# Optimization experiments

Measured on AMD Instinct MI355X. Metric: run time of the kernel, lower is better.

Reference implementation:

```python
import jax, jax.numpy as jnp
import numpy as np

T = 4  # message-passing steps (hparams['T'])
D = 64  # link_state_dim
RU = 256  # readout_units


def setup_inputs() -> dict:
    key = jax.random.key(0)
    ks = jax.random.split(key, 12)
    num_edges = 100000
    n_pairs = 1600000
    link_state = jax.random.normal(ks[0], (num_edges, D), dtype=jnp.float32)
    first_critic = jax.random.randint(ks[1], (n_pairs,), 0, num_edges)
    second_critic = jax.random.randint(ks[2], (n_pairs,), 0, num_edges)
    s = 0.05
    return {
        'link_state': link_state,
        'first_critic': first_critic,
        'second_critic': second_critic,
        'num_edges_critic': num_edges,
        'W_msg': jax.random.normal(ks[3], (2 * D, D), dtype=jnp.float32) * s,
        'b_msg': jnp.zeros((D,), dtype=jnp.float32),
        'gru_kernel': jax.random.normal(ks[4], (D, 3 * D), dtype=jnp.float32) * s,
        'gru_rkernel': jax.random.normal(ks[5], (D, 3 * D), dtype=jnp.float32) * s,
        'gru_bias': jnp.zeros((2, 3 * D), dtype=jnp.float32),  # reset_after=True: [input_bias, recurrent_bias]
        'W1': jax.random.normal(ks[6], (D, RU), dtype=jnp.float32) * s,
        'b1': jnp.zeros((RU,), dtype=jnp.float32),
        'W2': jax.random.normal(ks[7], (RU, RU), dtype=jnp.float32) * s,
        'b2': jnp.zeros((RU,), dtype=jnp.float32),
        'W3': jax.random.normal(ks[8], (RU, 1), dtype=jnp.float32) * s,
        'b3': jnp.zeros((1,), dtype=jnp.float32),
    }


def _gru_cell(x, h, kernel, rkernel, bias):
    # Keras GRUCell, reset_after=True
    mx = x @ kernel + bias[0]          # [E, 3D]
    mi = h @ rkernel + bias[1]         # [E, 3D]
    z = jax.nn.sigmoid(mx[:, :D] + mi[:, :D])
    r = jax.nn.sigmoid(mx[:, D:2 * D] + mi[:, D:2 * D])
    hh = jnp.tanh(mx[:, 2 * D:] + r * mi[:, 2 * D:])
    return z * h + (1.0 - z) * hh


def reference(link_state, first_critic, second_critic, num_edges_critic,
              W_msg, b_msg, gru_kernel, gru_rkernel, gru_bias,
              W1, b1, W2, b2, W3, b3):
    for _ in range(T):
        main_nodes = link_state[first_critic]        # [P, D] gather
        neigh_nodes = link_state[second_critic]      # [P, D] gather
        nodes_concat = jnp.concatenate([main_nodes, neigh_nodes], axis=1)  # [P, 2D]
        msg = jax.nn.selu(nodes_concat @ W_msg + b_msg)                    # [P, D]
        agg = jax.ops.segment_sum(msg, second_critic, num_segments=num_edges_critic)  # [E, D]
        link_state = _gru_cell(agg, link_state, gru_kernel, gru_rkernel, gru_bias)
    # tf.reduce_sum([link_state], axis=1): stack -> [1, E, D], sum over E -> [1, D]
    g = jnp.sum(link_state, axis=0, keepdims=True)   # [1, D]
    h1 = jax.nn.selu(g @ W1 + b1)
    h2 = jax.nn.selu(h1 @ W2 + b2)
    return h2 @ W3 + b3                              # [1, 1]
```

## Files before the change

### kernel.cpp

```cpp
#include <hip/hip_runtime.h>
#include <hip/hip_bf16.h>

#define D 64
#define TSTEPS 4

__device__ __forceinline__ float selu_f(float x) {
  const float sc = 1.0507009873554805f;
  const float scal = 1.7580993408473766f;
  return x > 0.f ? sc * x : scal * (__expf(x) - 1.f);
}
__device__ __forceinline__ float sigm_f(float x) {
  return 1.f / (1.f + __expf(-x));
}
__device__ __forceinline__ float tanh_f(float x) {
  return 1.f - 2.f / (__expf(2.f * x) + 1.f);
}
__device__ __forceinline__ unsigned short f2bf(float x) {
  union { float f; unsigned u; } v; v.f = x;
  unsigned r = v.u + 0x7fff + ((v.u >> 16) & 1);
  return (unsigned short)(r >> 16);
}
__device__ __forceinline__ float bf2f(unsigned short x) {
  union { unsigned u; float f; } v; v.u = ((unsigned)x) << 16;
  return v.f;
}

__global__ void k_setup(int* __restrict__ counts, float* __restrict__ g, int E) {
  for (int i = blockIdx.x * blockDim.x + threadIdx.x; i < E; i += gridDim.x * blockDim.x)
    counts[i] = 0;
  int t = blockIdx.x * blockDim.x + threadIdx.x;
  if (t < D) g[t] = 0.f;
}

__global__ void k_hist(const int* __restrict__ sec, int* counts, int P) {
  int i = blockIdx.x * blockDim.x + threadIdx.x;
  if (i < P) atomicAdd(&counts[sec[i]], 1);
}

__global__ void k_scan(const int* __restrict__ counts, int* __restrict__ offsets,
                       int* __restrict__ cursor, int E, int P) {
  __shared__ int lds[1024];
  int t = threadIdx.x;
  int per = (E + 1023) >> 10;
  int lo = t * per, hi = min(lo + per, E);
  int s = 0;
  for (int i = lo; i < hi; ++i) s += counts[i];
  lds[t] = s;
  __syncthreads();
  for (int d = 1; d < 1024; d <<= 1) {
    int v = (t >= d) ? lds[t - d] : 0;
    __syncthreads();
    lds[t] += v;
    __syncthreads();
  }
  int run = (t == 0) ? 0 : lds[t - 1];
  for (int i = lo; i < hi; ++i) {
    int c = counts[i];
    offsets[i] = run;
    cursor[i] = run;
    run += c;
  }
  if (t == 1023) offsets[E] = P;
}

__global__ void k_scatter(const int* __restrict__ fst, const int* __restrict__ sec,
                          int* cursor, int* __restrict__ sorted_first, int P) {
  int i = blockIdx.x * blockDim.x + threadIdx.x;
  if (i < P) {
    int e = sec[i];
    int pos = atomicAdd(&cursor[e], 1);
    sorted_first[pos] = fst[i];
  }
}

__global__ void k_prep(const float* __restrict__ Wmsg,
                       const float* __restrict__ gk, const float* __restrict__ grk,
                       const float* __restrict__ gb,
                       float* __restrict__ Wuv, float* __restrict__ Wg, float* __restrict__ bg) {
  int i = blockIdx.x * blockDim.x + threadIdx.x;
  if (i < 64 * 128) {
    int k = i >> 7, c = i & 127;
    Wuv[i] = (c < 64) ? Wmsg[k * 64 + c] : Wmsg[(64 + k) * 64 + (c - 64)];
  }
  if (i < 128 * 256) {
    int r = i >> 8, c = i & 255;
    float v;
    if (r < 64) {
      v = (c < 192) ? gk[r * 192 + c] : 0.f;
    } else {
      int rr = r - 64;
      if (c < 128) v = grk[rr * 192 + c];
      else if (c < 192) v = 0.f;
      else v = grk[rr * 192 + (c - 64)];
    }
    Wg[i] = v;
  }
  if (i < 256) {
    float v;
    if (i < 128) v = gb[i] + gb[192 + i];
    else if (i < 192) v = gb[i];
    else v = gb[i + 128];
    bg[i] = v;
  }
}

template <int UV16>
__global__ __launch_bounds__(256) void k_uv(const float* __restrict__ h,
                                            const float* __restrict__ Wuv,
                                            const float* __restrict__ bmsg,
                                            void* __restrict__ UVp, int E) {
  __shared__ float As[32 * 65];
  int t = threadIdx.x;
  int base = blockIdx.x * 32;
  for (int q = t; q < 32 * 16; q += 256) {
    int row = q >> 4, k4 = (q & 15) << 2;
    float4 v = make_float4(0.f, 0.f, 0.f, 0.f);
    if (base + row < E)
      v = *reinterpret_cast<const float4*>(h + (size_t)(base + row) * 64 + k4);
    As[row * 65 + k4 + 0] = v.x;
    As[row * 65 + k4 + 1] = v.y;
    As[row * 65 + k4 + 2] = v.z;
    As[row * 65 + k4 + 3] = v.w;
  }
  __syncthreads();
  int ct = t & 31, eg = t >> 5;
  int c0 = ct * 4;
  float4 binit = make_float4(0.f, 0.f, 0.f, 0.f);
  if (c0 >= 64) binit = *reinterpret_cast<const float4*>(bmsg + (c0 - 64));
  float4 acc[4];
  acc[0] = binit; acc[1] = binit; acc[2] = binit; acc[3] = binit;
#pragma unroll 8
  for (int k = 0; k < 64; ++k) {
    float4 bv = *reinterpret_cast<const float4*>(Wuv + k * 128 + c0);
#pragma unroll
    for (int j = 0; j < 4; ++j) {
      float a = As[(eg + j * 8) * 65 + k];
      acc[j].x += a * bv.x; acc[j].y += a * bv.y;
      acc[j].z += a * bv.z; acc[j].w += a * bv.w;
    }
  }
#pragma unroll
  for (int j = 0; j < 4; ++j) {
    int e = base + eg + j * 8;
    if (e < E) {
      if constexpr (UV16) {
        ushort4 s;
        s.x = f2bf(acc[j].x); s.y = f2bf(acc[j].y);
        s.z = f2bf(acc[j].z); s.w = f2bf(acc[j].w);
        *reinterpret_cast<ushort4*>((unsigned short*)UVp + (size_t)e * 128 + c0) = s;
      } else {
        *reinterpret_cast<float4*>((float*)UVp + (size_t)e * 128 + c0) = acc[j];
      }
    }
  }
}

template <int UV16, int AGG16>
__global__ __launch_bounds__(256) void k_pair(const void* __restrict__ UVp,
                                              const int* __restrict__ offsets,
                                              const int* __restrict__ sorted_first,
                                              void* __restrict__ aggp, int E) {
  int w = (blockIdx.x << 2) + (threadIdx.x >> 6);
  if (w >= E) return;
  int c = threadIdx.x & 63;
  const float* UV32 = (const float*)UVp;
  const unsigned short* UV16p = (const unsigned short*)UVp;
  float base;
  if constexpr (UV16) base = bf2f(UV16p[(size_t)w * 128 + 64 + c]);
  else                base = UV32[(size_t)w * 128 + 64 + c];
  int i = offsets[w], end = offsets[w + 1];
  float acc = 0.f;
  for (; i + 3 < end; i += 4) {
    int f0 = sorted_first[i];
    int f1 = sorted_first[i + 1];
    int f2 = sorted_first[i + 2];
    int f3 = sorted_first[i + 3];
    float u0, u1, u2, u3;
    if constexpr (UV16) {
      u0 = bf2f(UV16p[(size_t)f0 * 128 + c]);
      u1 = bf2f(UV16p[(size_t)f1 * 128 + c]);
      u2 = bf2f(UV16p[(size_t)f2 * 128 + c]);
      u3 = bf2f(UV16p[(size_t)f3 * 128 + c]);
    } else {
      u0 = UV32[(size_t)f0 * 128 + c];
      u1 = UV32[(size_t)f1 * 128 + c];
      u2 = UV32[(size_t)f2 * 128 + c];
      u3 = UV32[(size_t)f3 * 128 + c];
    }
    acc += selu_f(u0 + base);
    acc += selu_f(u1 + base);
    acc += selu_f(u2 + base);
    acc += selu_f(u3 + base);
  }
  for (; i < end; ++i) {
    int f0 = sorted_first[i];
    float u;
    if constexpr (UV16) u = bf2f(UV16p[(size_t)f0 * 128 + c]);
    else                u = UV32[(size_t)f0 * 128 + c];
    acc += selu_f(u + base);
  }
  if constexpr (AGG16)
    ((unsigned short*)aggp)[(size_t)w * 64 + c] = f2bf(acc);
  else
    ((float*)aggp)[(size_t)w * 64 + c] = acc;
}

template <int UV16, int AGG16>
__global__ __launch_bounds__(256) void k_gru(const void* __restrict__ aggp,
                                             const float* __restrict__ h_in,
                                             float* __restrict__ h_out,
                                             const float* __restrict__ Wg,
                                             const float* __restrict__ bg,
                                             const float* __restrict__ Wuv,
                                             const float* __restrict__ bmsg,
                                             void* __restrict__ UVp,
                                             float* __restrict__ g,
                                             int E, int write_uv, int accum_g) {
  __shared__ float As[32 * 129];
  __shared__ float Ms[32 * 257];
  __shared__ float red[256];
  int t = threadIdx.x;
  int base = blockIdx.x * 32;

  for (int q = t; q < 32 * 32; q += 256) {
    int row = q >> 5, c4 = (q & 31) << 2;
    int e = base + row;
    float4 v = make_float4(0.f, 0.f, 0.f, 0.f);
    if (e < E) {
      if (c4 < 64) {
        if constexpr (AGG16) {
          ushort4 s = *reinterpret_cast<const ushort4*>(
              (const unsigned short*)aggp + (size_t)e * 64 + c4);
          v = make_float4(bf2f(s.x), bf2f(s.y), bf2f(s.z), bf2f(s.w));
        } else {
          v = *reinterpret_cast<const float4*>((const float*)aggp + (size_t)e * 64 + c4);
        }
      } else {
        v = *reinterpret_cast<const float4*>(h_in + (size_t)e * 64 + (c4 - 64));
      }
    }
    As[row * 129 + c4 + 0] = v.x;
    As[row * 129 + c4 + 1] = v.y;
    As[row * 129 + c4 + 2] = v.z;
    As[row * 129 + c4 + 3] = v.w;
  }
  __syncthreads();

  {
    int wv = t >> 6;
    int lane = t & 63;
    int ct8 = lane & 7;
    int rg = lane >> 3;
    int c0 = wv * 64 + ct8 * 8;
    int kbeg = (wv == 3) ? 64 : 0;
    int kend = (wv == 2) ? 64 : 128;
    float4 b0 = *reinterpret_cast<const float4*>(bg + c0);
    float4 b1 = *reinterpret_cast<const float4*>(bg + c0 + 4);
    float4 acc0[4], acc1[4];
#pragma unroll
    for (int j = 0; j < 4; ++j) { acc0[j] = b0; acc1[j] = b1; }
#pragma unroll 4
    for (int k = kbeg; k < kend; ++k) {
      float4 bv0 = *reinterpret_cast<const float4*>(Wg + k * 256 + c0);
      float4 bv1 = *reinterpret_cast<const float4*>(Wg + k * 256 + c0 + 4);
#pragma unroll
      for (int j = 0; j < 4; ++j) {
        float a = As[(rg + j * 8) * 129 + k];
        acc0[j].x += a * bv0.x; acc0[j].y += a * bv0.y;
        acc0[j].z += a * bv0.z; acc0[j].w += a * bv0.w;
        acc1[j].x += a * bv1.x; acc1[j].y += a * bv1.y;
        acc1[j].z += a * bv1.z; acc1[j].w += a * bv1.w;
      }
    }
#pragma unroll
    for (int j = 0; j < 4; ++j) {
      float* m = Ms + (rg + j * 8) * 257 + c0;
      m[0] = acc0[j].x; m[1] = acc0[j].y; m[2] = acc0[j].z; m[3] = acc0[j].w;
      m[4] = acc1[j].x; m[5] = acc1[j].y; m[6] = acc1[j].z; m[7] = acc1[j].w;
    }
  }
  __syncthreads();

  float gsum = 0.f;
#pragma unroll
  for (int j = 0; j < 8; ++j) {
    int u = t + 256 * j;
    int e = u >> 6, c = u & 63;
    int ge = base + e;
    float mz = Ms[e * 257 + c];
    float mr = Ms[e * 257 + 64 + c];
    float mx2 = Ms[e * 257 + 128 + c];
    float mi2 = Ms[e * 257 + 192 + c];
    float hold = As[e * 129 + 64 + c];
    float z = sigm_f(mz);
    float r = sigm_f(mr);
    float hh = tanh_f(mx2 + r * mi2);
    float hn = z * hold + (1.f - z) * hh;
    if (ge < E) {
      h_out[(size_t)ge * 64 + c] = hn;
    } else {
      hn = 0.f;
    }
    As[e * 129 + 64 + c] = hn;
    gsum += hn;
  }
  __syncthreads();

  if (write_uv) {
    int ct = t & 31, eg = t >> 5;
    int c0 = ct * 4;
    float4 binit = make_float4(0.f, 0.f, 0.f, 0.f);
    if (c0 >= 64) binit = *reinterpret_cast<const float4*>(bmsg + (c0 - 64));
    float4 acc[4];
    acc[0] = binit; acc[1] = binit; acc[2] = binit; acc[3] = binit;
#pragma unroll 8
    for (int k = 0; k < 64; ++k) {
      float4 bv = *reinterpret_cast<const float4*>(Wuv + k * 128 + c0);
#pragma unroll
      for (int j = 0; j < 4; ++j) {
        float a = As[(eg + j * 8) * 129 + 64 + k];
        acc[j].x += a * bv.x; acc[j].y += a * bv.y;
        acc[j].z += a * bv.z; acc[j].w += a * bv.w;
      }
    }
#pragma unroll
    for (int j = 0; j < 4; ++j) {
      int e = base + eg + j * 8;
      if (e < E) {
        if constexpr (UV16) {
          ushort4 s;
          s.x = f2bf(acc[j].x); s.y = f2bf(acc[j].y);
          s.z = f2bf(acc[j].z); s.w = f2bf(acc[j].w);
          *reinterpret_cast<ushort4*>((unsigned short*)UVp + (size_t)e * 128 + c0) = s;
        } else {
          *reinterpret_cast<float4*>((float*)UVp + (size_t)e * 128 + c0) = acc[j];
        }
      }
    }
  }

  if (accum_g) {
    red[t] = gsum;
    __syncthreads();
    if (t < 64) atomicAdd(&g[t], red[t] + red[t + 64] + red[t + 128] + red[t + 192]);
  }
}

__global__ __launch_bounds__(256) void k_mlp(const float* __restrict__ g,
                                             const float* __restrict__ W1, const float* __restrict__ b1,
                                             const float* __restrict__ W2, const float* __restrict__ b2,
                                             const float* __restrict__ W3, const float* __restrict__ b3,
                                             float* __restrict__ out) {
  __shared__ float gs[64];
  __shared__ float h1[256];
  __shared__ float h2[256];
  __shared__ float red[256];
  int t = threadIdx.x;
  if (t < 64) gs[t] = g[t];
  __syncthreads();
  float acc = b1[t];
#pragma unroll
  for (int k = 0; k < 64; ++k) acc += gs[k] * W1[k * 256 + t];
  h1[t] = selu_f(acc);
  __syncthreads();
  acc = b2[t];
#pragma unroll 8
  for (int k = 0; k < 256; ++k) acc += h1[k] * W2[k * 256 + t];
  h2[t] = selu_f(acc);
  __syncthreads();
  red[t] = h2[t] * W3[t];
  __syncthreads();
  for (int d = 128; d > 0; d >>= 1) {
    if (t < d) red[t] += red[t + d];
    __syncthreads();
  }
  if (t == 0) out[0] = red[0] + b3[0];
}

extern "C" void kernel_launch(void* const* d_in, const int* in_sizes, int n_in,
                              void* d_out, int out_size, void* d_ws, size_t ws_size,
                              hipStream_t stream) {
  const float* ls   = (const float*)d_in[0];
  const int*   fst  = (const int*)d_in[1];
  const int*   sec  = (const int*)d_in[2];
  const float* Wmsg = (const float*)d_in[4];
  const float* bmsg = (const float*)d_in[5];
  const float* gk   = (const float*)d_in[6];
  const float* grk  = (const float*)d_in[7];
  const float* gb   = (const float*)d_in[8];
  const float* W1   = (const float*)d_in[9];
  const float* b1   = (const float*)d_in[10];
  const float* W2   = (const float*)d_in[11];
  const float* b2   = (const float*)d_in[12];
  const float* W3   = (const float*)d_in[13];
  const float* b3   = (const float*)d_in[14];
  int E = in_sizes[0] / D;
  int P = in_sizes[1];
  float* out = (float*)d_out;
  (void)n_in; (void)out_size;

  auto total_need = [&](int uv16, int agg16) -> size_t {
    size_t o = 0;
    auto add = [&](size_t b) { o = (o + b + 255) & ~(size_t)255; };
    add((size_t)E * 64 * 4);
    add((size_t)E * 128 * (uv16 ? 2 : 4));
    add((size_t)E * 64 * (agg16 ? 2 : 4));
    add(((size_t)E + 1) * 4);
    add((size_t)E * 4);
    add((size_t)P * 4);
    add(64 * 128 * 4);
    add(128 * 256 * 4);
    add(256 * 4);
    add(64 * 4);
    return o;
  };
  int uv16 = 0, agg16 = 0;
  if (total_need(0, 0) > ws_size) { uv16 = 1; }
  if (uv16 && total_need(1, 0) > ws_size) { agg16 = 1; }

  char* ws = (char*)d_ws;
  size_t off = 0;
  auto alloc = [&](size_t bytes) {
    void* p = ws + off;
    off = (off + bytes + 255) & ~(size_t)255;
    return p;
  };
  float* h            = (float*)alloc((size_t)E * 64 * 4);
  void*  UV           = alloc((size_t)E * 128 * (uv16 ? 2 : 4));
  void*  agg          = alloc((size_t)E * 64 * (agg16 ? 2 : 4));
  int*   offsets      = (int*)alloc(((size_t)E + 1) * 4);
  int*   counts       = (int*)alloc((size_t)E * 4);
  int*   cursor       = counts;
  int*   sorted_first = (int*)alloc((size_t)P * 4);
  float* Wuv          = (float*)alloc(64 * 128 * 4);
  float* Wg           = (float*)alloc(128 * 256 * 4);
  float* bg           = (float*)alloc(256 * 4);
  float* g            = (float*)alloc(64 * 4);

  k_setup<<<512, 256, 0, stream>>>(counts, g, E);
  k_hist<<<(P + 255) / 256, 256, 0, stream>>>(sec, counts, P);
  k_scan<<<1, 1024, 0, stream>>>(counts, offsets, cursor, E, P);
  k_scatter<<<(P + 255) / 256, 256, 0, stream>>>(fst, sec, cursor, sorted_first, P);
  k_prep<<<128, 256, 0, stream>>>(Wmsg, gk, grk, gb, Wuv, Wg, bg);

  int gemm_blocks = (E + 31) / 32;
  int pair_blocks = (E + 3) / 4;

  if (!uv16) {
    k_uv<0><<<gemm_blocks, 256, 0, stream>>>(ls, Wuv, bmsg, UV, E);
    for (int it = 0; it < TSTEPS; ++it) {
      const float* hin = (it == 0) ? ls : h;
      int last = (it == TSTEPS - 1);
      k_pair<0, 0><<<pair_blocks, 256, 0, stream>>>(UV, offsets, sorted_first, agg, E);
      k_gru<0, 0><<<gemm_blocks, 256, 0, stream>>>(agg, hin, h, Wg, bg, Wuv, bmsg, UV, g,
                                                   E, !last, last);
    }
  } else if (!agg16) {
    k_uv<1><<<gemm_blocks, 256, 0, stream>>>(ls, Wuv, bmsg, UV, E);
    for (int it = 0; it < TSTEPS; ++it) {
      const float* hin = (it == 0) ? ls : h;
      int last = (it == TSTEPS - 1);
      k_pair<1, 0><<<pair_blocks, 256, 0, stream>>>(UV, offsets, sorted_first, agg, E);
      k_gru<1, 0><<<gemm_blocks, 256, 0, stream>>>(agg, hin, h, Wg, bg, Wuv, bmsg, UV, g,
                                                   E, !last, last);
    }
  } else {
    k_uv<1><<<gemm_blocks, 256, 0, stream>>>(ls, Wuv, bmsg, UV, E);
    for (int it = 0; it < TSTEPS; ++it) {
      const float* hin = (it == 0) ? ls : h;
      int last = (it == TSTEPS - 1);
      k_pair<1, 1><<<pair_blocks, 256, 0, stream>>>(UV, offsets, sorted_first, agg, E);
      k_gru<1, 1><<<gemm_blocks, 256, 0, stream>>>(agg, hin, h, Wg, bg, Wuv, bmsg, UV, g,
                                                   E, !last, last);
    }
  }
  k_mlp<<<1, 256, 0, stream>>>(g, W1, b1, W2, b2, W3, b3, out);
}
```

Baseline: 1.349 ms.

## Fuse pair aggregation into GRU kernel, parallelize scan, force bf16 UV

Adds a fused kernel that computes each block's segment-summed messages straight into shared memory and then runs the GRU and next-step UV projection, with UV double-buffered across steps so the separate agg buffer and per-step pair kernel launch go away. The single-block serial scan becomes a three-pass multi-block scan, and wave-uniform indices are marked with readfirstlane so they live in scalar registers. UV and agg are now always stored as bf16 instead of choosing by workspace size, which lowers precision in the fp32 cases. The last step skips writing h, and a memset replaces the setup kernel. The fused kernel uses about 50KB of shared memory per block and leaves one wave per edge row, which may reduce occupancy and latency hiding for the random gathers.

```diff
diff --git a/kernel.cpp b/kernel.cpp
--- a/kernel.cpp
+++ b/kernel.cpp
@@ -25,42 +25,81 @@
   return v.f;
 }
 
-__global__ void k_setup(int* __restrict__ counts, float* __restrict__ g, int E) {
-  for (int i = blockIdx.x * blockDim.x + threadIdx.x; i < E; i += gridDim.x * blockDim.x)
-    counts[i] = 0;
-  int t = blockIdx.x * blockDim.x + threadIdx.x;
-  if (t < D) g[t] = 0.f;
-}
-
 __global__ void k_hist(const int* __restrict__ sec, int* counts, int P) {
   int i = blockIdx.x * blockDim.x + threadIdx.x;
   if (i < P) atomicAdd(&counts[sec[i]], 1);
 }
 
-__global__ void k_scan(const int* __restrict__ counts, int* __restrict__ offsets,
-                       int* __restrict__ cursor, int E, int P) {
+__global__ __launch_bounds__(256) void k_scan1(const int* __restrict__ counts,
+                                               int* __restrict__ bsums, int E) {
+  __shared__ int red[256];
+  int b = blockIdx.x, t = threadIdx.x;
+  int i0 = b * 1024 + t * 4;
+  int s = 0;
+  if (i0 + 3 < E) {
+    int4 v = *reinterpret_cast<const int4*>(counts + i0);
+    s = v.x + v.y + v.z + v.w;
+  } else {
+#pragma unroll
+    for (int j = 0; j < 4; ++j) { int i = i0 + j; if (i < E) s += counts[i]; }
+  }
+  red[t] = s;
+  __syncthreads();
+  for (int d = 128; d > 0; d >>= 1) {
+    if (t < d) red[t] += red[t + d];
+    __syncthreads();
+  }
+  if (t == 0) bsums[b] = red[0];
+}
+
+__global__ __launch_bounds__(1024) void k_scan2(int* __restrict__ bsums, int NB) {
   __shared__ int lds[1024];
   int t = threadIdx.x;
-  int per = (E + 1023) >> 10;
-  int lo = t * per, hi = min(lo + per, E);
+  lds[t] = (t < NB) ? bsums[t] : 0;
+  __syncthreads();
+  for (int d = 1; d < 1024; d <<= 1) {
+    int u = (t >= d) ? lds[t - d] : 0;
+    __syncthreads();
+    lds[t] += u;
+    __syncthreads();
+  }
+  if (t < NB) bsums[t] = (t == 0) ? 0 : lds[t - 1];
+}
+
+__global__ __launch_bounds__(256) void k_scan3(const int* __restrict__ counts,
+                                               const int* __restrict__ bsums,
+                                               int* __restrict__ offsets,
+                                               int* __restrict__ cursor, int E, int P) {
+  __shared__ int red[256];
+  int b = blockIdx.x, t = threadIdx.x;
+  int i0 = b * 1024 + t * 4;
+  int c[4];
   int s = 0;
-  for (int i = lo; i < hi; ++i) s += counts[i];
-  lds[t] = s;
-  __syncthreads();
-  for (int d = 1; d < 1024; d <<= 1) {
-    int v = (t >= d) ? lds[t - d] : 0;
-    __syncthreads();
-    lds[t] += v;
-    __syncthreads();
-  }
-  int run = (t == 0) ? 0 : lds[t - 1];
-  for (int i = lo; i < hi; ++i) {
-    int c = counts[i];
-    offsets[i] = run;
-    cursor[i] = run;
-    run += c;
-  }
-  if (t == 1023) offsets[E] = P;
+#pragma unroll
+  for (int j = 0; j < 4; ++j) {
+    int i = i0 + j;
+    c[j] = (i < E) ? counts[i] : 0;
+    s += c[j];
+  }
+  red[t] = s;
+  __syncthreads();
+  for (int d = 1; d < 256; d <<= 1) {
+    int u = (t >= d) ? red[t - d] : 0;
+    __syncthreads();
+    red[t] += u;
+    __syncthreads();
+  }
+  int base = bsums[b] + ((t == 0) ? 0 : red[t - 1]);
+#pragma unroll
+  for (int j = 0; j < 4; ++j) {
+    int i = i0 + j;
+    if (i < E) {
+      offsets[i] = base;
+      cursor[i] = base;
+      base += c[j];
+    }
+  }
+  if (b == 0 && t == 0) offsets[E] = P;
 }
 
 __global__ void k_scatter(const int* __restrict__ fst, const int* __restrict__ sec,
@@ -104,11 +143,10 @@
   }
 }
 
-template <int UV16>
 __global__ __launch_bounds__(256) void k_uv(const float* __restrict__ h,
                                             const float* __restrict__ Wuv,
                                             const float* __restrict__ bmsg,
-                                            void* __restrict__ UVp, int E) {
+                                            unsigned short* __restrict__ UVp, int E) {
   __shared__ float As[32 * 65];
   int t = threadIdx.x;
   int base = blockIdx.x * 32;
@@ -143,77 +181,50 @@
   for (int j = 0; j < 4; ++j) {
     int e = base + eg + j * 8;
     if (e < E) {
-      if constexpr (UV16) {
-        ushort4 s;
-        s.x = f2bf(acc[j].x); s.y = f2bf(acc[j].y);
-        s.z = f2bf(acc[j].z); s.w = f2bf(acc[j].w);
-        *reinterpret_cast<ushort4*>((unsigned short*)UVp + (size_t)e * 128 + c0) = s;
-      } else {
-        *reinterpret_cast<float4*>((float*)UVp + (size_t)e * 128 + c0) = acc[j];
-      }
-    }
-  }
-}
-
-template <int UV16, int AGG16>
-__global__ __launch_bounds__(256) void k_pair(const void* __restrict__ UVp,
+      ushort4 s;
+      s.x = f2bf(acc[j].x); s.y = f2bf(acc[j].y);
+      s.z = f2bf(acc[j].z); s.w = f2bf(acc[j].w);
+      *reinterpret_cast<ushort4*>(UVp + (size_t)e * 128 + c0) = s;
+    }
+  }
+}
+
+__global__ __launch_bounds__(256) void k_pair(const unsigned short* __restrict__ UVp,
                                               const int* __restrict__ offsets,
                                               const int* __restrict__ sorted_first,
-                                              void* __restrict__ aggp, int E) {
+                                              unsigned short* __restrict__ aggp, int E) {
   int w = (blockIdx.x << 2) + (threadIdx.x >> 6);
   if (w >= E) return;
   int c = threadIdx.x & 63;
-  const float* UV32 = (const float*)UVp;
-  const unsigned short* UV16p = (const unsigned short*)UVp;
-  float base;
-  if constexpr (UV16) base = bf2f(UV16p[(size_t)w * 128 + 64 + c]);
-  else                base = UV32[(size_t)w * 128 + 64 + c];
-  int i = offsets[w], end = offsets[w + 1];
+  float base = bf2f(UVp[(size_t)w * 128 + 64 + c]);
+  int i = __builtin_amdgcn_readfirstlane(offsets[w]);
+  int end = __builtin_amdgcn_readfirstlane(offsets[w + 1]);
   float acc = 0.f;
   for (; i + 3 < end; i += 4) {
-    int f0 = sorted_first[i];
-    int f1 = sorted_first[i + 1];
-    int f2 = sorted_first[i + 2];
-    int f3 = sorted_first[i + 3];
-    float u0, u1, u2, u3;
-    if constexpr (UV16) {
-      u0 = bf2f(UV16p[(size_t)f0 * 128 + c]);
-      u1 = bf2f(UV16p[(size_t)f1 * 128 + c]);
-      u2 = bf2f(UV16p[(size_t)f2 * 128 + c]);
-      u3 = bf2f(UV16p[(size_t)f3 * 128 + c]);
-    } else {
-      u0 = UV32[(size_t)f0 * 128 + c];
-      u1 = UV32[(size_t)f1 * 128 + c];
-      u2 = UV32[(size_t)f2 * 128 + c];
-      u3 = UV32[(size_t)f3 * 128 + c];
-    }
-    acc += selu_f(u0 + base);
-    acc += selu_f(u1 + base);
-    acc += selu_f(u2 + base);
-    acc += selu_f(u3 + base);
+    int f0 = __builtin_amdgcn_readfirstlane(sorted_first[i]);
+    int f1 = __builtin_amdgcn_readfirstlane(sorted_first[i + 1]);
+    int f2 = __builtin_amdgcn_readfirstlane(sorted_first[i + 2]);
+    int f3 = __builtin_amdgcn_readfirstlane(sorted_first[i + 3]);
+    acc += selu_f(bf2f(UVp[(size_t)f0 * 128 + c]) + base);
+    acc += selu_f(bf2f(UVp[(size_t)f1 * 128 + c]) + base);
+    acc += selu_f(bf2f(UVp[(size_t)f2 * 128 + c]) + base);
+    acc += selu_f(bf2f(UVp[(size_t)f3 * 128 + c]) + base);
   }
   for (; i < end; ++i) {
-    int f0 = sorted_first[i];
-    float u;
-    if constexpr (UV16) u = bf2f(UV16p[(size_t)f0 * 128 + c]);
-    else                u = UV32[(size_t)f0 * 128 + c];
-    acc += selu_f(u + base);
-  }
-  if constexpr (AGG16)
-    ((unsigned short*)aggp)[(size_t)w * 64 + c] = f2bf(acc);
-  else
-    ((float*)aggp)[(size_t)w * 64 + c] = acc;
-}
-
-template <int UV16, int AGG16>
-__global__ __launch_bounds__(256) void k_gru(const void* __restrict__ aggp,
+    int f0 = __builtin_amdgcn_readfirstlane(sorted_first[i]);
+    acc += selu_f(bf2f(UVp[(size_t)f0 * 128 + c]) + base);
+  }
+  aggp[(size_t)w * 64 + c] = f2bf(acc);
+}
+
+__global__ __launch_bounds__(256) void k_gru(const unsigned short* __restrict__ aggp,
                                              const float* __restrict__ h_in,
                                              float* __restrict__ h_out,
                                              const float* __restrict__ Wg,
                                              const float* __restrict__ bg,
                                              const float* __restrict__ Wuv,
                                              const float* __restrict__ bmsg,
-                                             void* __restrict__ UVp,
+                                             unsigned short* __restrict__ UVp,
                                              float* __restrict__ g,
                                              int E, int write_uv, int accum_g) {
   __shared__ float As[32 * 129];
@@ -228,13 +239,8 @@
     float4 v = make_float4(0.f, 0.f, 0.f, 0.f);
     if (e < E) {
       if (c4 < 64) {
-        if constexpr (AGG16) {
-          ushort4 s = *reinterpret_cast<const ushort4*>(
-              (const unsigned short*)aggp + (size_t)e * 64 + c4);
-          v = make_float4(bf2f(s.x), bf2f(s.y), bf2f(s.z), bf2f(s.w));
-        } else {
-          v = *reinterpret_cast<const float4*>((const float*)aggp + (size_t)e * 64 + c4);
-        }
+        ushort4 s = *reinterpret_cast<const ushort4*>(aggp + (size_t)e * 64 + c4);
+        v = make_float4(bf2f(s.x), bf2f(s.y), bf2f(s.z), bf2f(s.w));
       } else {
         v = *reinterpret_cast<const float4*>(h_in + (size_t)e * 64 + (c4 - 64));
       }
@@ -297,7 +303,7 @@
     float hh = tanh_f(mx2 + r * mi2);
     float hn = z * hold + (1.f - z) * hh;
     if (ge < E) {
-      h_out[(size_t)ge * 64 + c] = hn;
+      if (!accum_g) h_out[(size_t)ge * 64 + c] = hn;
     } else {
       hn = 0.f;
     }
@@ -327,14 +333,165 @@
     for (int j = 0; j < 4; ++j) {
       int e = base + eg + j * 8;
       if (e < E) {
-        if constexpr (UV16) {
-          ushort4 s;
-          s.x = f2bf(acc[j].x); s.y = f2bf(acc[j].y);
-          s.z = f2bf(acc[j].z); s.w = f2bf(acc[j].w);
-          *reinterpret_cast<ushort4*>((unsigned short*)UVp + (size_t)e * 128 + c0) = s;
-        } else {
-          *reinterpret_cast<float4*>((float*)UVp + (size_t)e * 128 + c0) = acc[j];
+        ushort4 s;
+        s.x = f2bf(acc[j].x); s.y = f2bf(acc[j].y);
+        s.z = f2bf(acc[j].z); s.w = f2bf(acc[j].w);
+        *reinterpret_cast<ushort4*>(UVp + (size_t)e * 128 + c0) = s;
+      }
+    }
+  }
+
+  if (accum_g) {
+    red[t] = gsum;
+    __syncthreads();
+    if (t < 64) atomicAdd(&g[t], red[t] + red[t + 64] + red[t + 128] + red[t + 192]);
+  }
+}
+
+__global__ __launch_bounds__(256) void k_fused(const unsigned short* __restrict__ UVin,
+                                               const int* __restrict__ offsets,
+                                               const int* __restrict__ sorted_first,
+                                               const float* __restrict__ h_in,
+                                               float* __restrict__ h_out,
+                                               const float* __restrict__ Wg,
+                                               const float* __restrict__ bg,
+                                               const float* __restrict__ Wuv,
+                                               const float* __restrict__ bmsg,
+                                               unsigned short* __restrict__ UVout,
+                                               float* __restrict__ g,
+                                               int E, int write_uv, int accum_g) {
+  __shared__ float As[32 * 129];
+  __shared__ float Ms[32 * 257];
+  __shared__ float red[256];
+  int t = threadIdx.x;
+  int base = blockIdx.x * 32;
+
+  for (int q = t; q < 32 * 16; q += 256) {
+    int row = q >> 4, c4 = (q & 15) << 2;
+    int e = base + row;
+    float4 v = make_float4(0.f, 0.f, 0.f, 0.f);
+    if (e < E) v = *reinterpret_cast<const float4*>(h_in + (size_t)e * 64 + c4);
+    As[row * 129 + 64 + c4 + 0] = v.x;
+    As[row * 129 + 64 + c4 + 1] = v.y;
+    As[row * 129 + 64 + c4 + 2] = v.z;
+    As[row * 129 + 64 + c4 + 3] = v.w;
+  }
+
+  {
+    int wv = t >> 6, c = t & 63;
+    for (int j = 0; j < 8; ++j) {
+      int row = wv * 8 + j;
+      int e = base + row;
+      float acc = 0.f;
+      if (e < E) {
+        float vb = bf2f(UVin[(size_t)e * 128 + 64 + c]);
+        int i = __builtin_amdgcn_readfirstlane(offsets[e]);
+        int end = __builtin_amdgcn_readfirstlane(offsets[e + 1]);
+        for (; i + 3 < end; i += 4) {
+          int f0 = __builtin_amdgcn_readfirstlane(sorted_first[i]);
+          int f1 = __builtin_amdgcn_readfirstlane(sorted_first[i + 1]);
+          int f2 = __builtin_amdgcn_readfirstlane(sorted_first[i + 2]);
+          int f3 = __builtin_amdgcn_readfirstlane(sorted_first[i + 3]);
+          acc += selu_f(bf2f(UVin[(size_t)f0 * 128 + c]) + vb);
+          acc += selu_f(bf2f(UVin[(size_t)f1 * 128 + c]) + vb);
+          acc += selu_f(bf2f(UVin[(size_t)f2 * 128 + c]) + vb);
+          acc += selu_f(bf2f(UVin[(size_t)f3 * 128 + c]) + vb);
         }
+        for (; i < end; ++i) {
+          int f0 = __builtin_amdgcn_readfirstlane(sorted_first[i]);
+          acc += selu_f(bf2f(UVin[(size_t)f0 * 128 + c]) + vb);
+        }
+      }
+      As[row * 129 + c] = acc;
+    }
+  }
+  __syncthreads();
+
+  {
+    int wv = t >> 6;
+    int lane = t & 63;
+    int ct8 = lane & 7;
+    int rg = lane >> 3;
+    int c0 = wv * 64 + ct8 * 8;
+    int kbeg = (wv == 3) ? 64 : 0;
+    int kend = (wv == 2) ? 64 : 128;
+    float4 b0 = *reinterpret_cast<const float4*>(bg + c0);
+    float4 b1 = *reinterpret_cast<const float4*>(bg + c0 + 4);
+    float4 acc0[4], acc1[4];
+#pragma unroll
+    for (int j = 0; j < 4; ++j) { acc0[j] = b0; acc1[j] = b1; }
+#pragma unroll 4
+    for (int k = kbeg; k < kend; ++k) {
+      float4 bv0 = *reinterpret_cast<const float4*>(Wg + k * 256 + c0);
+      float4 bv1 = *reinterpret_cast<const float4*>(Wg + k * 256 + c0 + 4);
+#pragma unroll
+      for (int j = 0; j < 4; ++j) {
+        float a = As[(rg + j * 8) * 129 + k];
+        acc0[j].x += a * bv0.x; acc0[j].y += a * bv0.y;
+        acc0[j].z += a * bv0.z; acc0[j].w += a * bv0.w;
+        acc1[j].x += a * bv1.x; acc1[j].y += a * bv1.y;
+        acc1[j].z += a * bv1.z; acc1[j].w += a * bv1.w;
+      }
+    }
+#pragma unroll
+    for (int j = 0; j < 4; ++j) {
+      float* m = Ms + (rg + j * 8) * 257 + c0;
+      m[0] = acc0[j].x; m[1] = acc0[j].y; m[2] = acc0[j].z; m[3] = acc0[j].w;
+      m[4] = acc1[j].x; m[5] = acc1[j].y; m[6] = acc1[j].z; m[7] = acc1[j].w;
+    }
+  }
+  __syncthreads();
+
+  float gsum = 0.f;
+#pragma unroll
+  for (int j = 0; j < 8; ++j) {
+    int u = t + 256 * j;
+    int e = u >> 6, c = u & 63;
+    int ge = base + e;
+    float mz = Ms[e * 257 + c];
+    float mr = Ms[e * 257 + 64 + c];
+    float mx2 = Ms[e * 257 + 128 + c];
+    float mi2 = Ms[e * 257 + 192 + c];
+    float hold = As[e * 129 + 64 + c];
+    float z = sigm_f(mz);
+    float r = sigm_f(mr);
+    float hh = tanh_f(mx2 + r * mi2);
+    float hn = z * hold + (1.f - z) * hh;
+    if (ge < E) {
+      if (!accum_g) h_out[(size_t)ge * 64 + c] = hn;
+    } else {
+      hn = 0.f;
+    }
+    As[e * 129 + 64 + c] = hn;
+    gsum += hn;
+  }
+  __syncthreads();
+
+  if (write_uv) {
+    int ct = t & 31, eg = t >> 5;
+    int c0 = ct * 4;
+    float4 binit = make_float4(0.f, 0.f, 0.f, 0.f);
+    if (c0 >= 64) binit = *reinterpret_cast<const float4*>(bmsg + (c0 - 64));
+    float4 acc[4];
+    acc[0] = binit; acc[1] = binit; acc[2] = binit; acc[3] = binit;
+#pragma unroll 8
+    for (int k = 0; k < 64; ++k) {
+      float4 bv = *reinterpret_cast<const float4*>(Wuv + k * 128 + c0);
+#pragma unroll
+      for (int j = 0; j < 4; ++j) {
+        float a = As[(eg + j * 8) * 129 + 64 + k];
+        acc[j].x += a * bv.x; acc[j].y += a * bv.y;
+        acc[j].z += a * bv.z; acc[j].w += a * bv.w;
+      }
+    }
+#pragma unroll
+    for (int j = 0; j < 4; ++j) {
+      int e = base + eg + j * 8;
+      if (e < E) {
+        ushort4 s;
+        s.x = f2bf(acc[j].x); s.y = f2bf(acc[j].y);
+        s.z = f2bf(acc[j].z); s.w = f2bf(acc[j].w);
+        *reinterpret_cast<ushort4*>(UVout + (size_t)e * 128 + c0) = s;
       }
     }
   }
@@ -399,14 +556,18 @@
   float* out = (float*)d_out;
   (void)n_in; (void)out_size;
 
-  auto total_need = [&](int uv16, int agg16) -> size_t {
+  int NB = (E + 1023) / 1024;
+
+  auto total_need = [&](int fused) -> size_t {
     size_t o = 0;
     auto add = [&](size_t b) { o = (o + b + 255) & ~(size_t)255; };
     add((size_t)E * 64 * 4);
-    add((size_t)E * 128 * (uv16 ? 2 : 4));
-    add((size_t)E * 64 * (agg16 ? 2 : 4));
+    add((size_t)E * 128 * 2);
+    add(fused ? (size_t)E * 128 * 2
+              : (size_t)E * 64 * 2);
     add(((size_t)E + 1) * 4);
     add((size_t)E * 4);
+    add((size_t)NB * 4);
     add((size_t)P * 4);
     add(64 * 128 * 4);
     add(128 * 256 * 4);
@@ -414,9 +575,7 @@
     add(64 * 4);
     return o;
   };
-  int uv16 = 0, agg16 = 0;
-  if (total_need(0, 0) > ws_size) { uv16 = 1; }
-  if (uv16 && total_need(1, 0) > ws_size) { agg16 = 1; }
+  int fused = (total_need(1) <= ws_size) ? 1 : 0;
 
   char* ws = (char*)d_ws;
   size_t off = 0;
@@ -425,53 +584,53 @@
     off = (off + bytes + 255) & ~(size_t)255;
     return p;
   };
-  float* h            = (float*)alloc((size_t)E * 64 * 4);
-  void*  UV           = alloc((size_t)E * 128 * (uv16 ? 2 : 4));
-  void*  agg          = alloc((size_t)E * 64 * (agg16 ? 2 : 4));
+  float*          h     = (float*)alloc((size_t)E * 64 * 4);
+  unsigned short* UV0   = (unsigned short*)alloc((size_t)E * 128 * 2);
+  unsigned short* UV1   = nullptr;
+  unsigned short* aggb  = nullptr;
+  if (fused) UV1  = (unsigned short*)alloc((size_t)E * 128 * 2);
+  else       aggb = (unsigned short*)alloc((size_t)E * 64 * 2);
   int*   offsets      = (int*)alloc(((size_t)E + 1) * 4);
   int*   counts       = (int*)alloc((size_t)E * 4);
   int*   cursor       = counts;
+  int*   bsums        = (int*)alloc((size_t)NB * 4);
   int*   sorted_first = (int*)alloc((size_t)P * 4);
   float* Wuv          = (float*)alloc(64 * 128 * 4);
   float* Wg           = (float*)alloc(128 * 256 * 4);
   float* bg           = (float*)alloc(256 * 4);
   float* g            = (float*)alloc(64 * 4);
 
-  k_setup<<<512, 256, 0, stream>>>(counts, g, E);
+  hipMemsetAsync(counts, 0, (size_t)E * 4, stream);
+  hipMemsetAsync(g, 0, 64 * 4, stream);
   k_hist<<<(P + 255) / 256, 256, 0, stream>>>(sec, counts, P);
-  k_scan<<<1, 1024, 0, stream>>>(counts, offsets, cursor, E, P);
+  k_scan1<<<NB, 256, 0, stream>>>(counts, bsums, E);
+  k_scan2<<<1, 1024, 0, stream>>>(bsums, NB);
+  k_scan3<<<NB, 256, 0, stream>>>(counts, bsums, offsets, cursor, E, P);
   k_scatter<<<(P + 255) / 256, 256, 0, stream>>>(fst, sec, cursor, sorted_first, P);
   k_prep<<<128, 256, 0, stream>>>(Wmsg, gk, grk, gb, Wuv, Wg, bg);
 
   int gemm_blocks = (E + 31) / 32;
   int pair_blocks = (E + 3) / 4;
 
-  if (!uv16) {
-    k_uv<0><<<gemm_blocks, 256, 0, stream>>>(ls, Wuv, bmsg, UV, E);
+  k_uv<<<gemm_blocks, 256, 0, stream>>>(ls, Wuv, bmsg, UV0, E);
+  if (fused) {
+    unsigned short* UVa = UV0;
+    unsigned short* UVb = UV1;
     for (int it = 0; it < TSTEPS; ++it) {
       const float* hin = (it == 0) ? ls : h;
       int last = (it == TSTEPS - 1);
-      k_pair<0, 0><<<pair_blocks, 256, 0, stream>>>(UV, offsets, sorted_first, agg, E);
-      k_gru<0, 0><<<gemm_blocks, 256, 0, stream>>>(agg, hin, h, Wg, bg, Wuv, bmsg, UV, g,
-                                                   E, !last, last);
-    }
-  } else if (!agg16) {
-    k_uv<1><<<gemm_blocks, 256, 0, stream>>>(ls, Wuv, bmsg, UV, E);
+      k_fused<<<gemm_blocks, 256, 0, stream>>>(UVa, offsets, sorted_first, hin, h,
+                                               Wg, bg, Wuv, bmsg, UVb, g,
+                                               E, !last, last);
+      unsigned short* tmp = UVa; UVa = UVb; UVb = tmp;
+    }
+  } else {
     for (int it = 0; it < TSTEPS; ++it) {
       const float* hin = (it == 0) ? ls : h;
       int last = (it == TSTEPS - 1);
-      k_pair<1, 0><<<pair_blocks, 256, 0, stream>>>(UV, offsets, sorted_first, agg, E);
-      k_gru<1, 0><<<gemm_blocks, 256, 0, stream>>>(agg, hin, h, Wg, bg, Wuv, bmsg, UV, g,
-                                                   E, !last, last);
-    }
-  } else {
-    k_uv<1><<<gemm_blocks, 256, 0, stream>>>(ls, Wuv, bmsg, UV, E);
-    for (int it = 0; it < TSTEPS; ++it) {
-      const float* hin = (it == 0) ? ls : h;
-      int last = (it == TSTEPS - 1);
-      k_pair<1, 1><<<pair_blocks, 256, 0, stream>>>(UV, offsets, sorted_first, agg, E);
-      k_gru<1, 1><<<gemm_blocks, 256, 0, stream>>>(agg, hin, h, Wg, bg, Wuv, bmsg, UV, g,
-                                                   E, !last, last);
+      k_pair<<<pair_blocks, 256, 0, stream>>>(UV0, offsets, sorted_first, aggb, E);
+      k_gru<<<gemm_blocks, 256, 0, stream>>>(aggb, hin, h, Wg, bg, Wuv, bmsg, UV0, g,
+                                             E, !last, last);
     }
   }
   k_mlp<<<1, 256, 0, stream>>>(g, W1, b1, W2, b2, W3, b3, out);
```

Result: slower. 1.640 ms (+21.5%).
